# Kernel tuning notes

Hardware: AMD Instinct MI355X
Metric: run time of the kernel (lower is better)

The kernel has to match this reference:

```python
import jax, jax.numpy as jnp
import numpy as np

B, T, C, L = 32, 800, 5000, 100  # batch, frames, vocab(incl blank=0), max label len
NEG = -1e30  # log-zero surrogate (safe for logsumexp, avoids inf-inf NaNs)


def setup_inputs() -> dict:
    key = jax.random.key(0)
    k1, k2_, k3, k4 = jax.random.split(key, 4)
    # nnet_output is assumed to be log-softmax output of the acoustic model
    nnet_output = jax.nn.log_softmax(jax.random.normal(k1, (B, T, C), jnp.float32), axis=-1)
    targets = jax.random.randint(k2_, (B, L), 1, C).astype(jnp.int32)  # labels in [1, C)
    input_lengths = (T - jax.random.randint(k3, (B,), 0, T // 4)).astype(jnp.int32)
    target_lengths = (L - jax.random.randint(k4, (B,), 0, L // 4)).astype(jnp.int32)
    return dict(nnet_output=nnet_output, targets=targets,
                input_lengths=input_lengths, target_lengths=target_lengths)


def _ctc_tot_scores(log_probs, targets, input_lengths, target_lengths):
    """Log-semiring total score of the CTC numerator lattice per utterance.
    Equivalent to k2.intersect_dense(num_graphs, dense_fsa_vec).get_tot_scores(log_semiring=True).
    """
    Bb, Tt, Cc = log_probs.shape
    Ll = targets.shape[1]
    S = 2 * Ll + 1  # extended label sequence with interleaved blanks
    ext = jnp.zeros((Bb, S), targets.dtype).at[:, 1::2].set(targets)  # [B,S]
    # emission scores gathered along the extended labels: [B,T,S]
    emit = jnp.take_along_axis(log_probs, jnp.broadcast_to(ext[:, None, :], (Bb, Tt, S)), axis=2)
    emit_seq = jnp.transpose(emit, (1, 0, 2))  # [T,B,S]
    # skip transition s-2 -> s allowed iff ext[s] != blank and ext[s] != ext[s-2]
    ext_m2 = jnp.pad(ext[:, :-2], ((0, 0), (2, 0)), constant_values=-1)
    skip_ok = (ext != 0) & (ext != ext_m2)  # [B,S]

    alpha0 = jnp.full((Bb, S), NEG, log_probs.dtype)
    alpha0 = alpha0.at[:, 0].set(emit_seq[0, :, 0]).at[:, 1].set(emit_seq[0, :, 1])

    def step(alpha, emit_t):
        a1 = alpha
        a2 = jnp.pad(alpha[:, :-1], ((0, 0), (1, 0)), constant_values=NEG)
        a3 = jnp.where(skip_ok, jnp.pad(alpha[:, :-2], ((0, 0), (2, 0)), constant_values=NEG), NEG)
        m = jnp.maximum(jnp.maximum(a1, a2), a3)
        new = m + jnp.log(jnp.exp(a1 - m) + jnp.exp(a2 - m) + jnp.exp(a3 - m)) + emit_t
        return new, new

    _, alphas_rest = jax.lax.scan(step, alpha0, emit_seq[1:])
    alphas = jnp.concatenate([alpha0[None], alphas_rest], axis=0)  # [T,B,S]

    bidx = jnp.arange(Bb)
    final_alpha = alphas[input_lengths - 1, bidx, :]  # [B,S] alpha at last valid frame
    s_last = 2 * target_lengths       # final blank state
    s_prev = 2 * target_lengths - 1   # final label state
    tot = jnp.logaddexp(final_alpha[bidx, s_last], final_alpha[bidx, s_prev])  # [B]
    return tot


def reference(nnet_output, targets, input_lengths, target_lengths):
    tot_scores = _ctc_tot_scores(nnet_output, targets, input_lengths, target_lengths)
    finite = tot_scores > (NEG / 2)  # mirrors get_tot_objf_and_num_frames filtering -inf
    frames = input_lengths.astype(jnp.int64)
    tot_score = jnp.sum(jnp.where(finite, tot_scores, 0.0))
    tot_frames = jnp.sum(jnp.where(finite, frames, 0))
    all_frames = jnp.sum(frames)
    return (tot_score, tot_frames, all_frames)
```

## Files before the change

### kernel.cpp

```cpp
#include <hip/hip_runtime.h>


constexpr int B  = 32;
constexpr int T  = 800;
constexpr int C  = 5000;
constexpr int L  = 100;
constexpr int S  = 2 * L + 1;
constexpr int SP = 204;
constexpr int CH = 32;
constexpr int CHE = CH * SP;
constexpr int BLK = 320;
constexpr int NPROD = 256;
constexpr float NEGV = -1e30f;

__device__ __forceinline__ float lse2(float a, float b) {
    const float m = fmaxf(a, b);
    return m + __logf(__expf(a - m) + __expf(b - m));
}
__device__ __forceinline__ float lse3(float a, float b, float c) {
    const float m = fmaxf(a, fmaxf(b, c));
    return m + __logf(__expf(a - m) + __expf(b - m) + __expf(c - m));
}

__global__ __launch_bounds__(BLK) void ctc_fused(
    const float* __restrict__ lp, const int* __restrict__ targets,
    const int* __restrict__ il_, const int* __restrict__ tl_,
    float* __restrict__ out)
{
    __shared__ float buf[2][CHE];
    __shared__ int   tgt[L];
    __shared__ float sm[256];

    const int b   = blockIdx.x;
    const int tid = threadIdx.x;
    const int il  = il_[b];
    const int nch = (il + CH - 1) / CH;
    const float* __restrict__ base = lp + (size_t)b * T * C;

    if (tid < L) tgt[tid] = targets[b * L + tid];
    __syncthreads();

    const int lane = tid;
    const int s0   = 4 * lane;
    bool skip1 = false, skip3 = false;
    bool v0 = false, v1 = false, v2c = false, v3 = false;
    int  off = 0;
    if (tid < 64) {
        const int l2 = 2 * lane;
        const int i1 = (l2     < L) ? l2     : L - 1;
        const int i3 = (l2 + 1 < L) ? l2 + 1 : L - 1;
        const int ip = (l2 - 1 >= 0) ? l2 - 1 : 0;
        const int c1i = tgt[i1], c3i = tgt[i3], cpi = tgt[ip];
        skip1 = (lane == 0) ? true : (c1i != cpi);
        skip3 = (c3i != c1i);
        v0  = (s0     < S);
        v1  = (s0 + 1 < S);
        v2c = (s0 + 2 < S);
        v3  = (s0 + 3 < S);
        off = (s0 <= 200) ? s0 : 200;
    }

    float a0 = NEGV, a1v = NEGV, a2v = NEGV, a3v = NEGV;

    for (int c = -1; c < nch; ++c) {
        if (tid >= 64) {
            const int c2 = c + 1;
            if (c2 < nch) {
                float* dst = buf[c2 & 1];
                const int tbase = c2 * CH;
                const int pid = tid - 64;
#pragma unroll
                for (int bat = 0; bat < 2; ++bat) {
                    float v[13];
                    int   fl[13];
#pragma unroll
                    for (int j = 0; j < 13; ++j) {
                        const int flat = (bat * 13 + j) * NPROD + pid;
                        fl[j] = flat;
                        float val = NEGV;
                        if (flat < CHE) {
                            const int r = flat / SP;
                            const int s = flat - r * SP;
                            const int t = tbase + r;
                            if (t < il) {
                                const int cls = ((s & 1) && s < S) ? tgt[s >> 1] : 0;
                                val = base[(size_t)t * C + cls];
                            }
                        }
                        v[j] = val;
                    }
#pragma unroll
                    for (int j = 0; j < 13; ++j)
                        if (fl[j] < CHE) dst[fl[j]] = v[j];
                }
            }
        } else if (c >= 0) {
            const float* bp = buf[c & 1];
            const int tbase = c * CH;
            const int rmax  = (il - tbase < CH) ? (il - tbase) : CH;
            float4 e = *(const float4*)(bp + off);
            for (int r = 0; r < rmax; ++r) {
                const float4 cur = e;
                if (r + 1 < rmax) e = *(const float4*)(bp + (r + 1) * SP + off);
                const int t = tbase + r;
                if (t == 0) {
                    a0  = (lane == 0) ? cur.x : NEGV;
                    a1v = (lane == 0) ? cur.y : NEGV;
                    a2v = NEGV; a3v = NEGV;
                } else {
                    float up3 = __shfl_up(a3v, 1);
                    float up2 = __shfl_up(a2v, 1);
                    if (lane == 0) { up3 = NEGV; up2 = NEGV; }
                    const float n0 = lse2(a0, up3) + cur.x;
                    const float n1 = (skip1 ? lse3(a1v, a0, up3) : lse2(a1v, a0)) + cur.y;
                    const float n2 = lse2(a2v, a1v) + cur.z;
                    const float n3 = (skip3 ? lse3(a3v, a2v, a1v) : lse2(a3v, a2v)) + cur.w;
                    a0  = v0  ? n0 : NEGV;
                    a1v = v1  ? n1 : NEGV;
                    a2v = v2c ? n2 : NEGV;
                    a3v = v3  ? n3 : NEGV;
                }
            }
        }
        __syncthreads();
    }

    if (tid < 64) {
        sm[s0 + 0] = a0;
        sm[s0 + 1] = a1v;
        sm[s0 + 2] = a2v;
        sm[s0 + 3] = a3v;
    }
    __syncthreads();

    if (tid == 0) {
        const int tl = tl_[b];
        const float tot = lse2(sm[2 * tl], sm[2 * tl - 1]);
        const bool finite = tot > (NEGV * 0.5f);
        atomicAdd(out + 0, finite ? tot : 0.0f);
        atomicAdd(out + 1, finite ? (float)il : 0.0f);
        atomicAdd(out + 2, (float)il);
    }
}

extern "C" void kernel_launch(void* const* d_in, const int* in_sizes, int n_in,
                              void* d_out, int out_size, void* d_ws, size_t ws_size,
                              hipStream_t stream)
{
    const float* lp      = (const float*)d_in[0];
    const int*   targets = (const int*)d_in[1];
    const int*   il      = (const int*)d_in[2];
    const int*   tl      = (const int*)d_in[3];
    float* out = (float*)d_out;

    hipMemsetAsync(d_out, 0, (size_t)out_size * sizeof(float), stream);
    ctc_fused<<<B, BLK, 0, stream>>>(lp, targets, il, tl, out);
}
```

Baseline: 802.0 us.

## Split gather into a parallel pre-pass kernel writing compact emissions to workspace

Adds a separate gather kernel, launched over batch x time-chunks, that pulls the 101 distinct emission columns (100 labels plus blank) into a compact workspace of 104 floats per row. The alpha kernel then streams those rows into shared memory with plain float4 copies and reads the blank value once, instead of duplicating it across the 204-wide extended row. The scattered per-element gather from the 5000-wide rows used to run on only 32 blocks and stall the serial recursion; spreading it over many blocks is meant to hide that latency. The cost is a second launch and a workspace round trip, and the fused kernel stays as a fallback when the workspace is too small.

```diff
diff --git a/kernel.cpp b/kernel.cpp
--- a/kernel.cpp
+++ b/kernel.cpp
@@ -6,12 +6,15 @@
 constexpr int C  = 5000;
 constexpr int L  = 100;
 constexpr int S  = 2 * L + 1;
-constexpr int SP = 204;
-constexpr int CH = 32;
-constexpr int CHE = CH * SP;
+constexpr float NEGV = -1e30f;
+
+constexpr int RP  = 104;
+constexpr int CH  = 64;
+constexpr int CHE = CH * RP;
 constexpr int BLK = 320;
 constexpr int NPROD = 256;
-constexpr float NEGV = -1e30f;
+constexpr int GCH = 32;
+constexpr size_t WS_NEED = (size_t)B * T * RP * sizeof(float);
 
 __device__ __forceinline__ float lse2(float a, float b) {
     const float m = fmaxf(a, b);
@@ -22,8 +25,44 @@
     return m + __logf(__expf(a - m) + __expf(b - m) + __expf(c - m));
 }
 
-__global__ __launch_bounds__(BLK) void ctc_fused(
+__global__ __launch_bounds__(128) void ctc_gather(
     const float* __restrict__ lp, const int* __restrict__ targets,
+    const int* __restrict__ il_, float* __restrict__ ws)
+{
+    __shared__ int tgt[L];
+    const int b  = blockIdx.x;
+    const int t0 = blockIdx.y * GCH;
+    const int j  = threadIdx.x;
+    if (j < L) tgt[j] = targets[b * L + j];
+    __syncthreads();
+
+    const int il   = il_[b];
+    const int rows = ((il - t0) < GCH) ? (il - t0) : GCH;
+    if (rows <= 0 || j >= RP) return;
+
+    float* __restrict__ dst = ws + ((size_t)b * T + t0) * RP + j;
+
+    if (j > 100) {
+#pragma unroll
+        for (int i = 0; i < GCH; ++i)
+            if (i < rows) dst[(size_t)i * RP] = NEGV;
+        return;
+    }
+    const int cls = (j < 100) ? tgt[j] : 0;
+    const float* __restrict__ sp = lp + ((size_t)b * T + t0) * C + cls;
+
+    if (rows == GCH) {
+#pragma unroll 8
+        for (int i = 0; i < GCH; ++i)
+            dst[(size_t)i * RP] = sp[(size_t)i * C];
+    } else {
+        for (int i = 0; i < rows; ++i)
+            dst[(size_t)i * RP] = sp[(size_t)i * C];
+    }
+}
+
+__global__ __launch_bounds__(BLK) void ctc_alpha(
+    const float* __restrict__ ws, const int* __restrict__ targets,
     const int* __restrict__ il_, const int* __restrict__ tl_,
     float* __restrict__ out)
 {
@@ -35,6 +74,114 @@
     const int tid = threadIdx.x;
     const int il  = il_[b];
     const int nch = (il + CH - 1) / CH;
+    const float* __restrict__ base = ws + (size_t)b * T * RP;
+
+    if (tid < L) tgt[tid] = targets[b * L + tid];
+    __syncthreads();
+
+    const int lane = tid;
+    const int s0   = 4 * lane;
+    bool skip1 = false, skip3 = false;
+    bool v0 = false, v1 = false, v2c = false, v3 = false;
+    int  offt = 0;
+    if (tid < 64) {
+        const int l2 = 2 * lane;
+        const int i1 = (l2     < L) ? l2     : L - 1;
+        const int i3 = (l2 + 1 < L) ? l2 + 1 : L - 1;
+        const int ip = (l2 - 1 >= 0) ? l2 - 1 : 0;
+        const int c1i = tgt[i1], c3i = tgt[i3], cpi = tgt[ip];
+        skip1 = (lane == 0) ? true : (c1i != cpi);
+        skip3 = (c3i != c1i);
+        v0  = (s0     < S);
+        v1  = (s0 + 1 < S);
+        v2c = (s0 + 2 < S);
+        v3  = (s0 + 3 < S);
+        offt = (l2 <= 100) ? l2 : 100;
+    }
+
+    float a0 = NEGV, a1v = NEGV, a2v = NEGV, a3v = NEGV;
+
+    for (int c = -1; c < nch; ++c) {
+        if (tid >= 64) {
+            const int c2 = c + 1;
+            if (c2 < nch) {
+                const int rows = ((il - c2 * CH) < CH) ? (il - c2 * CH) : CH;
+                const int jmax = rows * (RP / 4);
+                float4* __restrict__ dst = (float4*)buf[c2 & 1];
+                const float4* __restrict__ src =
+                    (const float4*)(base + (size_t)c2 * CHE);
+                for (int j = tid - 64; j < jmax; j += NPROD) dst[j] = src[j];
+            }
+        } else if (c >= 0) {
+            const float* bp = buf[c & 1];
+            const int tbase = c * CH;
+            const int rmax  = (il - tbase < CH) ? (il - tbase) : CH;
+            float2 tv = *(const float2*)(bp + offt);
+            float  bl = bp[100];
+            for (int r = 0; r < rmax; ++r) {
+                const float2 ctv = tv;
+                const float  cbl = bl;
+                if (r + 1 < rmax) {
+                    tv = *(const float2*)(bp + (r + 1) * RP + offt);
+                    bl = bp[(r + 1) * RP + 100];
+                }
+                const int t = tbase + r;
+                if (t == 0) {
+                    a0  = (lane == 0) ? cbl   : NEGV;
+                    a1v = (lane == 0) ? ctv.x : NEGV;
+                    a2v = NEGV; a3v = NEGV;
+                } else {
+                    float up3 = __shfl_up(a3v, 1);
+                    if (lane == 0) up3 = NEGV;
+                    const float n0 = lse2(a0, up3) + cbl;
+                    const float n1 = (skip1 ? lse3(a1v, a0, up3) : lse2(a1v, a0)) + ctv.x;
+                    const float n2 = lse2(a2v, a1v) + cbl;
+                    const float n3 = (skip3 ? lse3(a3v, a2v, a1v) : lse2(a3v, a2v)) + ctv.y;
+                    a0  = v0  ? n0 : NEGV;
+                    a1v = v1  ? n1 : NEGV;
+                    a2v = v2c ? n2 : NEGV;
+                    a3v = v3  ? n3 : NEGV;
+                }
+            }
+        }
+        __syncthreads();
+    }
+
+    if (tid < 64) {
+        sm[s0 + 0] = a0;
+        sm[s0 + 1] = a1v;
+        sm[s0 + 2] = a2v;
+        sm[s0 + 3] = a3v;
+    }
+    __syncthreads();
+
+    if (tid == 0) {
+        const int tl = tl_[b];
+        const float tot = lse2(sm[2 * tl], sm[2 * tl - 1]);
+        const bool finite = tot > (NEGV * 0.5f);
+        atomicAdd(out + 0, finite ? tot : 0.0f);
+        atomicAdd(out + 1, finite ? (float)il : 0.0f);
+        atomicAdd(out + 2, (float)il);
+    }
+}
+
+constexpr int SPF  = 204;
+constexpr int CHF  = 32;
+constexpr int CHEF = CHF * SPF;
+
+__global__ __launch_bounds__(BLK) void ctc_fused(
+    const float* __restrict__ lp, const int* __restrict__ targets,
+    const int* __restrict__ il_, const int* __restrict__ tl_,
+    float* __restrict__ out)
+{
+    __shared__ float buf[2][CHEF];
+    __shared__ int   tgt[L];
+    __shared__ float sm[256];
+
+    const int b   = blockIdx.x;
+    const int tid = threadIdx.x;
+    const int il  = il_[b];
+    const int nch = (il + CHF - 1) / CHF;
     const float* __restrict__ base = lp + (size_t)b * T * C;
 
     if (tid < L) tgt[tid] = targets[b * L + tid];
@@ -67,7 +214,7 @@
             const int c2 = c + 1;
             if (c2 < nch) {
                 float* dst = buf[c2 & 1];
-                const int tbase = c2 * CH;
+                const int tbase = c2 * CHF;
                 const int pid = tid - 64;
 #pragma unroll
                 for (int bat = 0; bat < 2; ++bat) {
@@ -78,9 +225,9 @@
                         const int flat = (bat * 13 + j) * NPROD + pid;
                         fl[j] = flat;
                         float val = NEGV;
-                        if (flat < CHE) {
-                            const int r = flat / SP;
-                            const int s = flat - r * SP;
+                        if (flat < CHEF) {
+                            const int r = flat / SPF;
+                            const int s = flat - r * SPF;
                             const int t = tbase + r;
                             if (t < il) {
                                 const int cls = ((s & 1) && s < S) ? tgt[s >> 1] : 0;
@@ -91,17 +238,17 @@
                     }
 #pragma unroll
                     for (int j = 0; j < 13; ++j)
-                        if (fl[j] < CHE) dst[fl[j]] = v[j];
+                        if (fl[j] < CHEF) dst[fl[j]] = v[j];
                 }
             }
         } else if (c >= 0) {
             const float* bp = buf[c & 1];
-            const int tbase = c * CH;
-            const int rmax  = (il - tbase < CH) ? (il - tbase) : CH;
+            const int tbase = c * CHF;
+            const int rmax  = (il - tbase < CHF) ? (il - tbase) : CHF;
             float4 e = *(const float4*)(bp + off);
             for (int r = 0; r < rmax; ++r) {
                 const float4 cur = e;
-                if (r + 1 < rmax) e = *(const float4*)(bp + (r + 1) * SP + off);
+                if (r + 1 < rmax) e = *(const float4*)(bp + (r + 1) * SPF + off);
                 const int t = tbase + r;
                 if (t == 0) {
                     a0  = (lane == 0) ? cur.x : NEGV;
@@ -109,8 +256,7 @@
                     a2v = NEGV; a3v = NEGV;
                 } else {
                     float up3 = __shfl_up(a3v, 1);
-                    float up2 = __shfl_up(a2v, 1);
-                    if (lane == 0) { up3 = NEGV; up2 = NEGV; }
+                    if (lane == 0) up3 = NEGV;
                     const float n0 = lse2(a0, up3) + cur.x;
                     const float n1 = (skip1 ? lse3(a1v, a0, up3) : lse2(a1v, a0)) + cur.y;
                     const float n2 = lse2(a2v, a1v) + cur.z;
@@ -154,5 +300,12 @@
     float* out = (float*)d_out;
 
     hipMemsetAsync(d_out, 0, (size_t)out_size * sizeof(float), stream);
-    ctc_fused<<<B, BLK, 0, stream>>>(lp, targets, il, tl, out);
-}
+
+    if (ws_size >= WS_NEED) {
+        float* ws = (float*)d_ws;
+        ctc_gather<<<dim3(B, T / GCH), 128, 0, stream>>>(lp, targets, il, ws);
+        ctc_alpha<<<B, BLK, 0, stream>>>(ws, targets, il, tl, out);
+    } else {
+        ctc_fused<<<B, BLK, 0, stream>>>(lp, targets, il, tl, out);
+    }
+}
```

Result: slower. 884.2 us (+10.3%).
